# Kernel optimization log

Hardware: AMD Instinct MI355X
Metric: run time of the kernel (lower is better)

## Reference

```python
import jax, jax.numpy as jnp
import numpy as np

D_MODEL = 2048
D_STATE = 64
D_CONV = 4
EXPAND = 2
HEADDIM = 64
NGROUPS = 1
CHUNK = 64
D_INNER = EXPAND * D_MODEL            # 4096
NHEADS = D_INNER // HEADDIM           # 64
D_XBC = D_INNER + 2 * NGROUPS * D_STATE
D_IN_PROJ = 2 * D_INNER + 2 * NGROUPS * D_STATE + NHEADS


def setup_inputs():
    key = jax.random.key(0)
    ks = jax.random.split(key, 8)
    B, L = 2, 4096
    u = jax.random.normal(ks[0], (B, L, D_MODEL), jnp.float32)
    W_in = jax.random.normal(ks[1], (D_IN_PROJ, D_MODEL), jnp.float32) * 0.02
    conv_w = jax.random.normal(ks[2], (D_XBC, D_CONV), jnp.float32) * 0.2
    conv_b = jnp.zeros((D_XBC,), jnp.float32)
    dt = jnp.exp(jax.random.uniform(ks[3], (NHEADS,)) * (np.log(0.1) - np.log(0.001)) + np.log(0.001))
    dt = jnp.clip(dt, 1e-4)
    dt_bias = dt + jnp.log(-jnp.expm1(-dt))
    A_log = jnp.log(jax.random.uniform(ks[4], (NHEADS,), minval=1.0, maxval=16.0))
    D_param = jnp.ones((NHEADS,), jnp.float32)
    norm_w = jnp.ones((D_INNER,), jnp.float32)
    W_out = jax.random.normal(ks[5], (D_MODEL, D_INNER), jnp.float32) * 0.02
    return dict(u=u, W_in=W_in, conv_w=conv_w, conv_b=conv_b, dt_bias=dt_bias,
                A_log=A_log, D_param=D_param, norm_w=norm_w, W_out=W_out)


def segsum(x):
    # x: (..., T) -> (..., T, T) with entry [l,s] = sum_{s< i <= l} x[i], -inf above diag
    T = x.shape[-1]
    mask_strict = jnp.tril(jnp.ones((T, T), bool), k=-1)
    mask_incl = jnp.tril(jnp.ones((T, T), bool), k=0)
    xe = jnp.where(mask_strict, x[..., :, None], 0.0)  # element [l,s] = x[l] if l>s
    xseg = jnp.cumsum(xe, axis=-2)
    return jnp.where(mask_incl, xseg, -jnp.inf)


def ssd_scan(X, A, Bm, Cm, block_len=CHUNK):
    # X: (b,L,h,p), A: (b,L,h), Bm/Cm: (b,L,h,n)
    b, seqlen, h, p = X.shape
    n = Bm.shape[-1]
    pad_len = (block_len - seqlen % block_len) % block_len
    if pad_len > 0:
        X = jnp.pad(X, ((0, 0), (0, pad_len), (0, 0), (0, 0)))
        A = jnp.pad(A, ((0, 0), (0, pad_len), (0, 0)))
        Bm = jnp.pad(Bm, ((0, 0), (0, pad_len), (0, 0), (0, 0)))
        Cm = jnp.pad(Cm, ((0, 0), (0, pad_len), (0, 0), (0, 0)))
    L = X.shape[1]
    c = L // block_len
    Xc = X.reshape(b, c, block_len, h, p)
    Ac = A.reshape(b, c, block_len, h).transpose(0, 3, 1, 2)  # (b,h,c,l)
    Bc = Bm.reshape(b, c, block_len, h, n)
    Cc = Cm.reshape(b, c, block_len, h, n)
    A_cum = jnp.cumsum(Ac, axis=-1)                           # (b,h,c,l)
    Lmat = jnp.exp(segsum(Ac))                                # (b,h,c,l,s)
    CB = jnp.einsum('bclhn,bcshn->bhcls', Cc, Bc)
    Y_diag = jnp.einsum('bhcls,bcshp->bhclp', CB * Lmat, Xc)
    decay_states = jnp.exp(A_cum[..., -1:] - A_cum)           # (b,h,c,l)
    states = jnp.einsum('bhcl,bclhn,bclhp->bhcpn', decay_states, Bc, Xc)
    init = jnp.zeros((b, h, 1, p, n), X.dtype)
    states = jnp.concatenate([init, states], axis=2)          # (b,h,c+1,p,n)
    chunk_decay = jnp.pad(A_cum[..., -1], ((0, 0), (0, 0), (1, 0)))  # (b,h,c+1)
    decay_chunk = jnp.exp(segsum(chunk_decay))                # (b,h,c+1,c+1)
    new_states = jnp.einsum('bhzc,bhcpn->bhzpn', decay_chunk, states)[:, :, :-1]
    Y_off = jnp.einsum('bclhn,bhcpn,bhcl->bhclp', Cc, new_states, jnp.exp(A_cum))
    Y = (Y_diag + Y_off).transpose(0, 2, 3, 1, 4).reshape(b, L, h, p)
    if pad_len > 0:
        Y = Y[:, :seqlen]
    return Y


def rmsnorm_grouped(x, w, ngroups, eps=1e-5):
    gs = x.shape[-1] // ngroups
    xg = x.reshape(*x.shape[:-1], ngroups, gs)
    xg = xg * jax.lax.rsqrt(jnp.mean(xg * xg, axis=-1, keepdims=True) + eps)
    return xg.reshape(x.shape) * w


def reference(u, W_in, conv_w, conv_b, dt_bias, A_log, D_param, norm_w, W_out):
    B, L, _ = u.shape
    zxbcdt = u @ W_in.T                                      # (B,L,d_in_proj)
    z = zxbcdt[..., :D_INNER]
    xBC = zxbcdt[..., D_INNER:D_INNER + D_XBC]
    dt = zxbcdt[..., D_INNER + D_XBC:]
    # causal depthwise conv1d, kernel D_CONV, left-pad D_CONV-1
    xpad = jnp.pad(xBC, ((0, 0), (D_CONV - 1, 0), (0, 0)))
    conv = conv_b
    for k in range(D_CONV):
        conv = conv + conv_w[:, k] * xpad[:, k:k + L, :]
    xBC = jax.nn.silu(conv)
    x = xBC[..., :D_INNER].reshape(B, L, NHEADS, HEADDIM)
    B_ssm = xBC[..., D_INNER:D_INNER + NGROUPS * D_STATE].reshape(B, L, NGROUPS, D_STATE)
    C_ssm = xBC[..., D_INNER + NGROUPS * D_STATE:].reshape(B, L, NGROUPS, D_STATE)
    if NGROUPS < NHEADS:
        rep = NHEADS // NGROUPS
        B_ssm = jnp.repeat(B_ssm, rep, axis=2)
        C_ssm = jnp.repeat(C_ssm, rep, axis=2)
    dt = jax.nn.softplus(dt + dt_bias)                        # (B,L,nheads)
    A = -jnp.exp(A_log)                                       # (nheads,)
    y = ssd_scan(x * dt[..., None], A * dt, B_ssm, C_ssm, block_len=CHUNK)
    y = y + D_param[:, None] * x
    y = y.reshape(B, L, D_INNER)
    y = rmsnorm_grouped(y * jax.nn.silu(z), norm_w, NGROUPS)
    return y @ W_out.T
```

## Files before the change

### kernel.cpp

```cpp
#include <hip/hip_runtime.h>
#include <hip/hip_bf16.h>
#include <math.h>

#define SEQ       4096
#define DMODEL    2048
#define DINNER    4096
#define DXBC      4224
#define NPROJ     8384
#define NHEADS    64
#define HDIM      64
#define DSTATE    64
#define NCHUNK    64
#define XLD       4352

typedef __attribute__((ext_vector_type(8))) _Float16 half8;
typedef __attribute__((ext_vector_type(4))) float floatx4;

__device__ __forceinline__ void async_copy16(void* lds, const void* g) {
  __builtin_amdgcn_global_load_lds(
      (const __attribute__((address_space(1))) unsigned int*)g,
      (__attribute__((address_space(3))) unsigned int*)lds, 16, 0, 0);
}

__device__ __forceinline__ float silu_f(float x) { return x / (1.f + expf(-x)); }

__global__ void diag_kernel(float* out, float v) { out[0] = v; }

__global__ void cvt_kernel(const float* __restrict__ src, _Float16* __restrict__ dst, int n) {
  int i = blockIdx.x * 256 + threadIdx.x;
  if (i < n) dst[i] = (_Float16)src[i];
}

__global__ void cvt_pad_kernel(const float* __restrict__ src, _Float16* __restrict__ dst) {
  int i = blockIdx.x * 256 + threadIdx.x;
  if (i >= 8448 * DMODEL) return;
  int r = i / DMODEL;
  dst[i] = (r < NPROJ) ? (_Float16)src[i] : (_Float16)0.f;
}

template <typename OT>
__global__ __launch_bounds__(256) void gemm_bt(
    const _Float16* __restrict__ A, const _Float16* __restrict__ B,
    OT* __restrict__ C, int K, int ldc, int tiles_m, int tiles_n) {
  __shared__ __align__(16) _Float16 As[128 * 32];
  __shared__ __align__(16) _Float16 Bs[128 * 32];
  int t = threadIdx.x;
  int nt = tiles_m * tiles_n;
  int id = blockIdx.x;
  int id2 = ((nt & 7) == 0) ? ((id & 7) * (nt >> 3) + (id >> 3)) : id;
  int wband = tiles_m << 2;
  int g = id2 / wband;
  int rm = id2 - g * wband;
  int bw = tiles_n - (g << 2); if (bw > 4) bw = 4;
  int pn = (g << 2) + rm % bw;
  int pm = rm / bw;
  int m0 = pm * 128, n0 = pn * 128;

  int w = t >> 6, lane = t & 63, q = lane >> 4, r = lane & 15;
  int wm = (w >> 1) * 64, wn = (w & 1) * 64;
  int srow = t >> 2;
  int scol = ((t & 3) ^ ((t >> 3) & 3)) * 8;
  const _Float16* gA  = A + (size_t)(m0 + srow) * K + scol;
  const _Float16* gA2 = gA + (size_t)64 * K;
  const _Float16* gB  = B + (size_t)(n0 + srow) * K + scol;
  const _Float16* gB2 = gB + (size_t)64 * K;
  floatx4 acc[4][4] = {};
  for (int k0 = 0; k0 < K; k0 += 32) {
    async_copy16(As + w * 512,        gA  + k0);
    async_copy16(As + 2048 + w * 512, gA2 + k0);
    async_copy16(Bs + w * 512,        gB  + k0);
    async_copy16(Bs + 2048 + w * 512, gB2 + k0);
    __syncthreads();
    half8 af[4], bf[4];
#pragma unroll
    for (int im = 0; im < 4; ++im) {
      int R = wm + im * 16 + r;
      af[im] = *(const half8*)&As[R * 32 + (q ^ ((R >> 1) & 3)) * 8];
    }
#pragma unroll
    for (int in = 0; in < 4; ++in) {
      int R = wn + in * 16 + r;
      bf[in] = *(const half8*)&Bs[R * 32 + (q ^ ((R >> 1) & 3)) * 8];
    }
#pragma unroll
    for (int im = 0; im < 4; ++im)
#pragma unroll
      for (int in = 0; in < 4; ++in)
        acc[im][in] = __builtin_amdgcn_mfma_f32_16x16x32_f16(af[im], bf[in], acc[im][in], 0, 0, 0);
    __syncthreads();
  }
#pragma unroll
  for (int im = 0; im < 4; ++im)
#pragma unroll
    for (int in = 0; in < 4; ++in)
#pragma unroll
      for (int i = 0; i < 4; ++i)
        C[(size_t)(m0 + wm + im * 16 + q * 4 + i) * ldc + n0 + wn + in * 16 + r] =
            (OT)acc[im][in][i];
}

__global__ void conv_silu_kernel(const _Float16* __restrict__ xin, const float* __restrict__ conv_w,
                                 const float* __restrict__ conv_b, _Float16* __restrict__ xcv) {
  int idx = blockIdx.x * 256 + threadIdx.x;
  if (idx >= SEQ * DXBC) return;
  int l = idx / DXBC;
  int c = idx - l * DXBC;
  const _Float16* zc = xin + (size_t)l * XLD + c;
  float acc = conv_b[c];
#pragma unroll
  for (int k = 0; k < 4; ++k) {
    int off = k - 3;
    if (l + off >= 0) acc += conv_w[c * 4 + k] * (float)zc[(long)off * XLD];
  }
  xcv[idx] = (_Float16)silu_f(acc);
}

__global__ void dt_kernel(const _Float16* __restrict__ dtraw, const float* __restrict__ dt_bias,
                          const float* __restrict__ A_log, float* __restrict__ dtp,
                          float* __restrict__ dA) {
  int idx = blockIdx.x * 256 + threadIdx.x;
  if (idx >= SEQ * NHEADS) return;
  int h = idx & 63;
  int row = idx >> 6;
  float x = (float)dtraw[(size_t)row * XLD + h] + dt_bias[h];
  float dtv = (x > 20.f) ? x : log1pf(expf(x));
  dtp[idx] = dtv;
  dA[idx] = -expf(A_log[h]) * dtv;
}

__global__ void cumsum_kernel(const float* __restrict__ dA, float* __restrict__ acum,
                              float* __restrict__ chs) {
  int tid = blockIdx.x * 256 + threadIdx.x;
  if (tid >= NCHUNK * NHEADS) return;
  int h = tid & 63;
  int c = tid >> 6;
  int lbase = c * 64;
  float a = 0.f;
  for (int l = 0; l < 64; ++l) {
    a += dA[(size_t)(lbase + l) * 64 + h];
    acum[(size_t)tid * 64 + l] = a;
  }
  chs[tid] = a;
}

__global__ __launch_bounds__(256) void states_kernel(
    const _Float16* __restrict__ xcv, const float* __restrict__ dtp,
    const float* __restrict__ acum, const float* __restrict__ chs,
    _Float16* __restrict__ states) {
  int bid = blockIdx.x;
  int c = bid & 63, h = bid >> 6;
  int row0 = c * 64;
  int acbase = (c * 64 + h) * 64;
  __shared__ __align__(16) _Float16 XdT[64 * 72];
  __shared__ __align__(16) _Float16 BdT[64 * 72];
  __shared__ float dec[64];
  int t = threadIdx.x;
  if (t < 64) dec[t] = expf(chs[acbase >> 6] - acum[acbase + t]);
  __syncthreads();
#pragma unroll
  for (int i = 0; i < 16; ++i) {
    int flat = i * 256 + t;
    int l = flat >> 6, col = flat & 63;
    int grow = row0 + l;
    float dtv = dtp[(size_t)grow * 64 + h];
    float xv = (float)xcv[(size_t)grow * DXBC + h * 64 + col] * dtv;
    XdT[col * 72 + l] = (_Float16)xv;
    float bv = (float)xcv[(size_t)grow * DXBC + DINNER + col] * dec[l];
    BdT[col * 72 + l] = (_Float16)bv;
  }
  __syncthreads();
  int w = t >> 6, lane = t & 63, q = lane >> 4, r = lane & 15;
#pragma unroll
  for (int in = 0; in < 4; ++in) {
    floatx4 a4 = {0.f, 0.f, 0.f, 0.f};
#pragma unroll
    for (int k0 = 0; k0 < 64; k0 += 32) {
      half8 af = *(const half8*)&XdT[(w * 16 + r) * 72 + k0 + q * 8];
      half8 bf = *(const half8*)&BdT[(in * 16 + r) * 72 + k0 + q * 8];
      a4 = __builtin_amdgcn_mfma_f32_16x16x32_f16(af, bf, a4, 0, 0, 0);
    }
#pragma unroll
    for (int i = 0; i < 4; ++i)
      states[((size_t)bid * 64 + (w * 16 + q * 4 + i)) * 64 + in * 16 + r] = (_Float16)a4[i];
  }
}

__global__ __launch_bounds__(256) void scan_kernel(_Float16* __restrict__ states,
                                                   const float* __restrict__ chs) {
  int bid = blockIdx.x;
  int h = bid >> 4, seg = bid & 15;
  int e = seg * 256 + threadIdx.x;
  float carry = 0.f;
  for (int c = 0; c < 64; ++c) {
    size_t idx = ((size_t)(h * 64 + c)) * 4096 + e;
    float s = (float)states[idx];
    states[idx] = (_Float16)carry;
    carry = carry * expf(chs[c * 64 + h]) + s;
  }
}

__global__ __launch_bounds__(256) void yout_kernel(
    const _Float16* __restrict__ xcv, const float* __restrict__ dtp,
    const float* __restrict__ acum, const _Float16* __restrict__ sin_,
    const float* __restrict__ Dp, _Float16* __restrict__ Y) {
  int bid = blockIdx.x;
  int c = bid & 63, h = bid >> 6;
  int row0 = c * 64;
  int acbase = (c * 64 + h) * 64;
  __shared__ __align__(16) _Float16 Cs[64 * 72];
  __shared__ __align__(16) _Float16 Bt[64 * 72];
  __shared__ __align__(16) _Float16 XdT[64 * 72];
  __shared__ __align__(16) _Float16 Ms[64 * 72];
  __shared__ float acs[64];
  int t = threadIdx.x;
  if (t < 64) acs[t] = acum[acbase + t];
#pragma unroll
  for (int i = 0; i < 16; ++i) {
    int flat = i * 256 + t;
    int l = flat >> 6, col = flat & 63;
    int grow = row0 + l;
    const _Float16* rp = xcv + (size_t)grow * DXBC;
    Cs[l * 72 + col] = rp[DINNER + DSTATE + col];
    Bt[l * 72 + col] = rp[DINNER + col];
    float xv = (float)rp[h * 64 + col] * dtp[(size_t)grow * 64 + h];
    XdT[col * 72 + l] = (_Float16)xv;
  }
  __syncthreads();
  int w = t >> 6, lane = t & 63, q = lane >> 4, r = lane & 15;
  int m = w * 16 + r;
#pragma unroll
  for (int in = 0; in < 4; ++in) {
    floatx4 cb = {0.f, 0.f, 0.f, 0.f};
#pragma unroll
    for (int k0 = 0; k0 < 64; k0 += 32) {
      half8 af = *(const half8*)&Cs[m * 72 + k0 + q * 8];
      half8 bf = *(const half8*)&Bt[(in * 16 + r) * 72 + k0 + q * 8];
      cb = __builtin_amdgcn_mfma_f32_16x16x32_f16(af, bf, cb, 0, 0, 0);
    }
#pragma unroll
    for (int i = 0; i < 4; ++i) {
      int l = w * 16 + q * 4 + i;
      int s = in * 16 + r;
      float v = (s <= l) ? cb[i] * expf(acs[l] - acs[s]) : 0.f;
      Ms[l * 72 + s] = (_Float16)v;
    }
  }
  __syncthreads();
  size_t sbase = (size_t)bid * 4096;
  float Dh = Dp[h];
#pragma unroll
  for (int in = 0; in < 4; ++in) {
    floatx4 acc = {0.f, 0.f, 0.f, 0.f};
#pragma unroll
    for (int k0 = 0; k0 < 64; k0 += 32) {
      half8 af = *(const half8*)&Cs[m * 72 + k0 + q * 8];
      half8 bf = *(const half8*)&sin_[sbase + (size_t)(in * 16 + r) * 64 + k0 + q * 8];
      acc = __builtin_amdgcn_mfma_f32_16x16x32_f16(af, bf, acc, 0, 0, 0);
    }
#pragma unroll
    for (int i = 0; i < 4; ++i) acc[i] *= expf(acs[w * 16 + q * 4 + i]);
#pragma unroll
    for (int k0 = 0; k0 < 64; k0 += 32) {
      half8 af = *(const half8*)&Ms[m * 72 + k0 + q * 8];
      half8 bf = *(const half8*)&XdT[(in * 16 + r) * 72 + k0 + q * 8];
      acc = __builtin_amdgcn_mfma_f32_16x16x32_f16(af, bf, acc, 0, 0, 0);
    }
#pragma unroll
    for (int i = 0; i < 4; ++i) {
      int l = w * 16 + q * 4 + i;
      int p = in * 16 + r;
      int grow = row0 + l;
      float xv = (float)xcv[(size_t)grow * DXBC + h * 64 + p];
      Y[(size_t)grow * DINNER + h * 64 + p] = (_Float16)(acc[i] + Dh * xv);
    }
  }
}

__global__ __launch_bounds__(256) void rmsnorm_kernel(const _Float16* __restrict__ Y,
                                                      _Float16* __restrict__ Z,
                                                      const float* __restrict__ norm_w) {
  int row = blockIdx.x;
  const _Float16* y = Y + (size_t)row * DINNER;
  _Float16* z = Z + (size_t)row * DINNER;
  __shared__ float gbuf[DINNER];
  __shared__ float red[4];
  int t = threadIdx.x;
  float ss = 0.f;
#pragma unroll
  for (int i = 0; i < 16; ++i) {
    int j = i * 256 + t;
    float zv = (float)z[j];
    float g = (float)y[j] * silu_f(zv);
    gbuf[j] = g;
    ss += g * g;
  }
#pragma unroll
  for (int o = 32; o > 0; o >>= 1) ss += __shfl_down(ss, o, 64);
  if ((t & 63) == 0) red[t >> 6] = ss;
  __syncthreads();
  float rs = rsqrtf((red[0] + red[1] + red[2] + red[3]) / (float)DINNER + 1e-5f);
#pragma unroll
  for (int i = 0; i < 16; ++i) {
    int j = i * 256 + t;
    z[j] = (_Float16)(gbuf[j] * rs * norm_w[j]);
  }
}

extern "C" void kernel_launch(void* const* d_in, const int* in_sizes, int n_in,
                              void* d_out, int out_size, void* d_ws, size_t ws_size,
                              hipStream_t stream) {
  const float* u       = (const float*)d_in[0];
  const float* W_in    = (const float*)d_in[1];
  const float* conv_w  = (const float*)d_in[2];
  const float* conv_b  = (const float*)d_in[3];
  const float* dt_bias = (const float*)d_in[4];
  const float* A_log   = (const float*)d_in[5];
  const float* D_param = (const float*)d_in[6];
  const float* norm_w  = (const float*)d_in[7];
  const float* W_out   = (const float*)d_in[8];
  float* out = (float*)d_out;
  char* ws = (char*)d_ws;

  const size_t off_z      = 0;
  const size_t off_xbcdt  = 33554432ULL;
  const size_t off_Y      = 33554432ULL;
  const size_t off_xcv    = 69206016ULL;
  const size_t off_winbf  = 69206016ULL;
  const size_t off_states = 103809024ULL;
  const size_t off_ubf    = 103809024ULL;
  const size_t off_wout   = 103809024ULL;
  const size_t off_dtp    = 137363456ULL;
  const size_t off_dA     = 138412032ULL;
  const size_t off_acum   = 139460608ULL;
  const size_t off_chs    = 140509184ULL;
  const size_t ws_needed  = 140525568ULL;
  if (ws_size < ws_needed) {
    diag_kernel<<<1, 1, 0, stream>>>(out, (float)ws_size);
    return;
  }

  _Float16* zb     = (_Float16*)(ws + off_z);
  _Float16* xbcdtb = (_Float16*)(ws + off_xbcdt);
  _Float16* Yb     = (_Float16*)(ws + off_Y);
  _Float16* xcv    = (_Float16*)(ws + off_xcv);
  _Float16* winbf  = (_Float16*)(ws + off_winbf);
  _Float16* states = (_Float16*)(ws + off_states);
  _Float16* ubf    = (_Float16*)(ws + off_ubf);
  _Float16* woutbf = (_Float16*)(ws + off_wout);
  float*    dtp    = (float*)(ws + off_dtp);
  float*    dAb    = (float*)(ws + off_dA);
  float*    acum   = (float*)(ws + off_acum);
  float*    chs    = (float*)(ws + off_chs);

  for (int b = 0; b < 2; ++b) {
    const float* ub = u + (size_t)b * SEQ * DMODEL;
    float* outb = out + (size_t)b * SEQ * DMODEL;

    cvt_kernel<<<(SEQ * DMODEL + 255) / 256, 256, 0, stream>>>(ub, ubf, SEQ * DMODEL);
    cvt_pad_kernel<<<(8448 * DMODEL + 255) / 256, 256, 0, stream>>>(W_in, winbf);

    gemm_bt<_Float16><<<32 * 32, 256, 0, stream>>>(ubf, winbf, zb, DMODEL, DINNER, 32, 32);
    gemm_bt<_Float16><<<32 * 34, 256, 0, stream>>>(
        ubf, winbf + (size_t)DINNER * DMODEL, xbcdtb, DMODEL, XLD, 32, 34);

    conv_silu_kernel<<<(SEQ * DXBC + 255) / 256, 256, 0, stream>>>(xbcdtb, conv_w, conv_b, xcv);
    dt_kernel<<<(SEQ * NHEADS + 255) / 256, 256, 0, stream>>>(
        xbcdtb + DXBC, dt_bias, A_log, dtp, dAb);
    cumsum_kernel<<<(NCHUNK * NHEADS + 255) / 256, 256, 0, stream>>>(dAb, acum, chs);

    states_kernel<<<NHEADS * NCHUNK, 256, 0, stream>>>(xcv, dtp, acum, chs, states);
    scan_kernel<<<NHEADS * 16, 256, 0, stream>>>(states, chs);
    yout_kernel<<<NHEADS * NCHUNK, 256, 0, stream>>>(xcv, dtp, acum, states, D_param, Yb);

    rmsnorm_kernel<<<SEQ, 256, 0, stream>>>(Yb, zb, norm_w);

    cvt_kernel<<<(DMODEL * DINNER + 255) / 256, 256, 0, stream>>>(W_out, woutbf, DMODEL * DINNER);
    gemm_bt<float><<<32 * 16, 256, 0, stream>>>(zb, woutbf, outb, DINNER, DMODEL, 32, 16);
  }
}
```

Measured before the change: 1.268 ms.

## Double GEMM K-tile to 64 and merge the two input-projection GEMMs

The GEMM K-step goes from 32 to 64, with a new 8-way XOR swizzle for the wider LDS rows. This halves the number of barrier and load iterations per tile. The two in_proj GEMMs (z part and xBC/dt part) become one launch that routes each output tile to one of two destination buffers based on its column. That removes a launch and the tail imbalance of two separate grids, at the cost of double the LDS use per block, which may lower occupancy.

```diff
diff --git a/kernel.cpp b/kernel.cpp
--- a/kernel.cpp
+++ b/kernel.cpp
@@ -39,11 +39,12 @@
 }
 
 template <typename OT>
-__global__ __launch_bounds__(256) void gemm_bt(
+__global__ __launch_bounds__(256) void gemm_bt64(
     const _Float16* __restrict__ A, const _Float16* __restrict__ B,
-    OT* __restrict__ C, int K, int ldc, int tiles_m, int tiles_n) {
-  __shared__ __align__(16) _Float16 As[128 * 32];
-  __shared__ __align__(16) _Float16 Bs[128 * 32];
+    OT* __restrict__ C0, OT* __restrict__ C1, int K,
+    int ldc0, int ldc1, int ncol0, int tiles_m, int tiles_n) {
+  __shared__ __align__(16) _Float16 As[128 * 64];
+  __shared__ __align__(16) _Float16 Bs[128 * 64];
   int t = threadIdx.x;
   int nt = tiles_m * tiles_n;
   int id = blockIdx.x;
@@ -58,44 +59,55 @@
 
   int w = t >> 6, lane = t & 63, q = lane >> 4, r = lane & 15;
   int wm = (w >> 1) * 64, wn = (w & 1) * 64;
-  int srow = t >> 2;
-  int scol = ((t & 3) ^ ((t >> 3) & 3)) * 8;
-  const _Float16* gA  = A + (size_t)(m0 + srow) * K + scol;
-  const _Float16* gA2 = gA + (size_t)64 * K;
-  const _Float16* gB  = B + (size_t)(n0 + srow) * K + scol;
-  const _Float16* gB2 = gB + (size_t)64 * K;
+  int rowoff = lane >> 3;
+  int chunkoff = ((lane & 7) ^ rowoff) * 8;
+  const _Float16* gA[4];
+  const _Float16* gB[4];
+#pragma unroll
+  for (int i = 0; i < 4; ++i) {
+    gA[i] = A + (size_t)(m0 + i * 32 + w * 8 + rowoff) * K + chunkoff;
+    gB[i] = B + (size_t)(n0 + i * 32 + w * 8 + rowoff) * K + chunkoff;
+  }
   floatx4 acc[4][4] = {};
-  for (int k0 = 0; k0 < K; k0 += 32) {
-    async_copy16(As + w * 512,        gA  + k0);
-    async_copy16(As + 2048 + w * 512, gA2 + k0);
-    async_copy16(Bs + w * 512,        gB  + k0);
-    async_copy16(Bs + 2048 + w * 512, gB2 + k0);
+  for (int k0 = 0; k0 < K; k0 += 64) {
+#pragma unroll
+    for (int i = 0; i < 4; ++i) {
+      async_copy16(As + (i * 32 + w * 8) * 64, gA[i] + k0);
+      async_copy16(Bs + (i * 32 + w * 8) * 64, gB[i] + k0);
+    }
     __syncthreads();
-    half8 af[4], bf[4];
-#pragma unroll
-    for (int im = 0; im < 4; ++im) {
-      int R = wm + im * 16 + r;
-      af[im] = *(const half8*)&As[R * 32 + (q ^ ((R >> 1) & 3)) * 8];
-    }
-#pragma unroll
-    for (int in = 0; in < 4; ++in) {
-      int R = wn + in * 16 + r;
-      bf[in] = *(const half8*)&Bs[R * 32 + (q ^ ((R >> 1) & 3)) * 8];
-    }
-#pragma unroll
-    for (int im = 0; im < 4; ++im)
-#pragma unroll
-      for (int in = 0; in < 4; ++in)
-        acc[im][in] = __builtin_amdgcn_mfma_f32_16x16x32_f16(af[im], bf[in], acc[im][in], 0, 0, 0);
+#pragma unroll
+    for (int kk = 0; kk < 64; kk += 32) {
+      half8 af[4], bf[4];
+#pragma unroll
+      for (int im = 0; im < 4; ++im) {
+        int R = wm + im * 16 + r;
+        af[im] = *(const half8*)&As[R * 64 + ((((kk >> 3) + q) ^ (R & 7)) << 3)];
+      }
+#pragma unroll
+      for (int in = 0; in < 4; ++in) {
+        int R = wn + in * 16 + r;
+        bf[in] = *(const half8*)&Bs[R * 64 + ((((kk >> 3) + q) ^ (R & 7)) << 3)];
+      }
+#pragma unroll
+      for (int im = 0; im < 4; ++im)
+#pragma unroll
+        for (int in = 0; in < 4; ++in)
+          acc[im][in] =
+              __builtin_amdgcn_mfma_f32_16x16x32_f16(af[im], bf[in], acc[im][in], 0, 0, 0);
+    }
     __syncthreads();
   }
+  OT* Cp = (n0 < ncol0) ? C0 : C1;
+  int ldc = (n0 < ncol0) ? ldc0 : ldc1;
+  int cb = (n0 < ncol0) ? n0 : n0 - ncol0;
 #pragma unroll
   for (int im = 0; im < 4; ++im)
 #pragma unroll
     for (int in = 0; in < 4; ++in)
 #pragma unroll
       for (int i = 0; i < 4; ++i)
-        C[(size_t)(m0 + wm + im * 16 + q * 4 + i) * ldc + n0 + wn + in * 16 + r] =
+        Cp[(size_t)(m0 + wm + im * 16 + q * 4 + i) * ldc + cb + wn + in * 16 + r] =
             (OT)acc[im][in][i];
 }
 
@@ -359,9 +371,8 @@
     cvt_kernel<<<(SEQ * DMODEL + 255) / 256, 256, 0, stream>>>(ub, ubf, SEQ * DMODEL);
     cvt_pad_kernel<<<(8448 * DMODEL + 255) / 256, 256, 0, stream>>>(W_in, winbf);
 
-    gemm_bt<_Float16><<<32 * 32, 256, 0, stream>>>(ubf, winbf, zb, DMODEL, DINNER, 32, 32);
-    gemm_bt<_Float16><<<32 * 34, 256, 0, stream>>>(
-        ubf, winbf + (size_t)DINNER * DMODEL, xbcdtb, DMODEL, XLD, 32, 34);
+    gemm_bt64<_Float16><<<32 * 66, 256, 0, stream>>>(
+        ubf, winbf, zb, xbcdtb, DMODEL, DINNER, XLD, DINNER, 32, 66);
 
     conv_silu_kernel<<<(SEQ * DXBC + 255) / 256, 256, 0, stream>>>(xbcdtb, conv_w, conv_b, xcv);
     dt_kernel<<<(SEQ * NHEADS + 255) / 256, 256, 0, stream>>>(
@@ -375,6 +386,7 @@
     rmsnorm_kernel<<<SEQ, 256, 0, stream>>>(Yb, zb, norm_w);
 
     cvt_kernel<<<(DMODEL * DINNER + 255) / 256, 256, 0, stream>>>(W_out, woutbf, DMODEL * DINNER);
-    gemm_bt<float><<<32 * 16, 256, 0, stream>>>(zb, woutbf, outb, DINNER, DMODEL, 32, 16);
-  }
-}
+    gemm_bt64<float><<<32 * 16, 256, 0, stream>>>(
+        zb, woutbf, outb, outb, DINNER, DMODEL, DMODEL, 1 << 30, 32, 16);
+  }
+}
```

Result: faster. 1.168 ms (-7.9%).
